# Performance work log

Measured on AMD Instinct MI355X. Metric: run time of the kernel, lower is better.

## Reference

```python
import jax, jax.numpy as jnp
import numpy as np

N, D, K = 500000, 64, 1024


def setup_inputs() -> dict:
    key = jax.random.key(0)
    kx, kc = jax.random.split(key)
    x = jax.random.normal(kx, (N, D), dtype=jnp.float32)
    centers = jax.random.normal(kc, (K, D), dtype=jnp.float32)
    return {"x": x, "centers": centers}


def reference(x, centers):
    # KMeans.predict: ids = argmin_k cdist(x, centers).
    # sqrt is monotone, so argmin over squared distances is identical, and the
    # This avoids the N x K x D expansion; the N x K score matrix is the
    # memory-bound hot path a fused kernel would stream over.
    m2 = jnp.sum(centers * centers, axis=-1)          # [K]
    scores = m2[None, :] - 2.0 * (x @ centers.T)      # [N, K]
    ids = jnp.argmin(scores, axis=-1)                 # [N]
    return ids
```

## Files before the change

### kernel.cpp

```cpp
#include <hip/hip_runtime.h>
#include <hip/hip_bf16.h>


#define N_PTS 500000
#define DIM   64
#define K_CENT 1024
#define MARGIN 8.0e-3f

typedef _Float16 half8   __attribute__((ext_vector_type(8)));
typedef float    floatx16 __attribute__((ext_vector_type(16)));

__global__ void kmeans_m2pre(const float* __restrict__ centers,
                             double* __restrict__ m2d)
{
    const int c = blockIdx.x * 256 + threadIdx.x;
    if (c >= K_CENT) return;
    const float4* crow = (const float4*)(centers + (size_t)c * DIM);
    double s = 0.0;
    #pragma unroll
    for (int kc = 0; kc < 16; ++kc) {
        float4 v = crow[kc];
        double a = v.x, b = v.y, cc = v.z, d = v.w;
        s += a * a + b * b + cc * cc + d * d;
    }
    m2d[c] = s;
}

__launch_bounds__(512, 4)
__global__ void kmeans_pass1(const float* __restrict__ x,
                             const float* __restrict__ centers,
                             int* __restrict__ out,
                             int* __restrict__ counter,
                             int* __restrict__ ulist,
                             int capacity)
{
    __shared__ __align__(16) _Float16 ldsC[256 * 72];
    __shared__ float negm2[256];

    const int tid  = threadIdx.x;
    const int lane = tid & 63;
    const int wave = tid >> 6;
    const int col  = lane & 31;
    const int h    = lane >> 5;

    const int p  = blockIdx.x * 256 + wave * 32 + col;
    const int pc = p > N_PTS - 1 ? N_PTS - 1 : p;

    half8 bh[4], bl[4];
    {
        const float* xr = x + (size_t)pc * DIM + h * 8;
        #pragma unroll
        for (int c = 0; c < 4; ++c) {
            float4 f0 = *(const float4*)(xr + c * 16);
            float4 f1 = *(const float4*)(xr + c * 16 + 4);
            float v[8] = {f0.x, f0.y, f0.z, f0.w, f1.x, f1.y, f1.z, f1.w};
            half8 hi, lo;
            #pragma unroll
            for (int j = 0; j < 8; ++j) {
                _Float16 hj = (_Float16)v[j];
                hi[j] = hj;
                lo[j] = (_Float16)(v[j] - (float)hj);
            }
            bh[c] = hi; bl[c] = lo;
        }
    }

    float m1 = -3.0e38f, m2 = -3.0e38f;
    int   ctb = 0;

    for (int s = 0; s < 4; ++s) {
        __syncthreads();
        {
            const int c = tid >> 1, hh = tid & 1;
            const float* src = centers + (size_t)(s * 256 + c) * DIM + hh * 32;
            float ss = 0.f;
            #pragma unroll
            for (int g = 0; g < 4; ++g) {
                float4 f0 = *(const float4*)(src + g * 8);
                float4 f1 = *(const float4*)(src + g * 8 + 4);
                float v[8] = {f0.x, f0.y, f0.z, f0.w, f1.x, f1.y, f1.z, f1.w};
                half8 hi;
                #pragma unroll
                for (int j = 0; j < 8; ++j) {
                    ss = fmaf(v[j], v[j], ss);
                    hi[j] = (_Float16)v[j];
                }
                *(half8*)&ldsC[c * 72 + hh * 32 + g * 8] = hi;
            }
            float oss = __shfl_xor(ss, 1);
            if (hh == 0) negm2[c] = -0.5f * (ss + oss);
        }
        __syncthreads();

        for (int ctl = 0; ctl < 8; ++ctl) {
            const int ct = s * 8 + ctl;
            const float* nm = &negm2[ctl * 32 + 4 * h];
            float4 q0 = *(const float4*)(nm);
            float4 q1 = *(const float4*)(nm + 8);
            float4 q2 = *(const float4*)(nm + 16);
            float4 q3 = *(const float4*)(nm + 24);
            floatx16 acc;
            acc[0]=q0.x; acc[1]=q0.y; acc[2]=q0.z; acc[3]=q0.w;
            acc[4]=q1.x; acc[5]=q1.y; acc[6]=q1.z; acc[7]=q1.w;
            acc[8]=q2.x; acc[9]=q2.y; acc[10]=q2.z; acc[11]=q2.w;
            acc[12]=q3.x; acc[13]=q3.y; acc[14]=q3.z; acc[15]=q3.w;

            const _Float16* ap = &ldsC[(ctl * 32 + col) * 72 + h * 8];
            #pragma unroll
            for (int c = 0; c < 4; ++c) {
                half8 a = *(const half8*)(ap + c * 16);
                acc = __builtin_amdgcn_mfma_f32_32x32x16_f16(a, bh[c], acc, 0, 0, 0);
                acc = __builtin_amdgcn_mfma_f32_32x32x16_f16(a, bl[c], acc, 0, 0, 0);
            }

            float kk[16];
            #pragma unroll
            for (int i = 0; i < 16; ++i) {
                unsigned u = (__float_as_uint(acc[i]) & 0xFFFFFFF0u) | (unsigned)i;
                kk[i] = __uint_as_float(u);
            }
            float M8[8], S8[8];
            #pragma unroll
            for (int j = 0; j < 8; ++j) {
                M8[j] = fmaxf(kk[2*j], kk[2*j+1]);
                S8[j] = fminf(kk[2*j], kk[2*j+1]);
            }
            float M4[4], S4[4];
            #pragma unroll
            for (int j = 0; j < 4; ++j) {
                M4[j] = fmaxf(M8[2*j], M8[2*j+1]);
                S4[j] = fmaxf(fmaxf(fminf(M8[2*j], M8[2*j+1]), S8[2*j]), S8[2*j+1]);
            }
            float M2a[2], S2a[2];
            #pragma unroll
            for (int j = 0; j < 2; ++j) {
                M2a[j] = fmaxf(M4[2*j], M4[2*j+1]);
                S2a[j] = fmaxf(fmaxf(fminf(M4[2*j], M4[2*j+1]), S4[2*j]), S4[2*j+1]);
            }
            float M16 = fmaxf(M2a[0], M2a[1]);
            float S16 = fmaxf(fmaxf(fminf(M2a[0], M2a[1]), S2a[0]), S2a[1]);

            m2 = fmaxf(fmaxf(m2, S16), fminf(M16, m1));
            bool gt = M16 > m1;
            m1 = gt ? M16 : m1;
            ctb = gt ? ct : ctb;
        }
    }

    {
        unsigned u = __float_as_uint(m1);
        int reg = (int)(u & 15u);
        int row = (reg & 3) + 8 * (reg >> 2) + 4 * h;
        int cid = ctb * 32 + row;

        float o1 = __shfl_xor(m1, 32);
        float o2 = __shfl_xor(m2, 32);
        int  ocid = __shfl_xor(cid, 32);
        float nm2 = fmaxf(fmaxf(m2, o2), fminf(m1, o1));
        bool take = o1 > m1;
        float nm1 = take ? o1 : m1;
        int  ncid = take ? ocid : cid;

        if (h == 0 && p < N_PTS) {
            out[p] = ncid;
            if (nm1 - nm2 < MARGIN) {
                int slot = atomicAdd(counter, 1);
                if (slot < capacity) ulist[slot] = p;
            }
        }
    }
}

__launch_bounds__(256)
__global__ void kmeans_pass2(const float* __restrict__ x,
                             const float* __restrict__ centers,
                             const double* __restrict__ m2d,
                             int* __restrict__ out,
                             const int* __restrict__ counter,
                             const int* __restrict__ ulist,
                             int capacity)
{
    int count = *counter;
    if (count > capacity) count = capacity;

    const int tid   = threadIdx.x;
    const int lane  = tid & 63;
    const int q     = lane & 15;
    const int rg    = lane >> 4;
    const int waveg = (blockIdx.x * 256 + tid) >> 6;
    const int nwave = (gridDim.x * 256) >> 6;

    for (int u = waveg; u < count; u += nwave) {
        const int p = ulist[u];
        float4 xv = *(const float4*)(x + (size_t)p * DIM + q * 4);
        const double x0 = xv.x, x1 = xv.y, x2 = xv.z, x3 = xv.w;

        double bv = 1.0e300; int bi = 0;
        #pragma unroll 4
        for (int g = 0; g < 256; ++g) {
            const int row = g * 4 + rg;
            float4 cv = *(const float4*)(centers + (size_t)row * DIM + q * 4);
            double dot = (double)cv.x * x0 + (double)cv.y * x1
                       + (double)cv.z * x2 + (double)cv.w * x3;
            #pragma unroll
            for (int m = 1; m <= 8; m <<= 1)
                dot += __shfl_xor(dot, m);
            double s = m2d[row] - 2.0 * dot;
            if (s < bv || (s == bv && row < bi)) { bv = s; bi = row; }
        }
        #pragma unroll
        for (int m = 16; m <= 32; m <<= 1) {
            double ov = __shfl_xor(bv, m);
            int    oi = __shfl_xor(bi, m);
            if (ov < bv || (ov == bv && oi < bi)) { bv = ov; bi = oi; }
        }
        if (lane == 0) out[p] = bi;
    }
}

extern "C" void kernel_launch(void* const* d_in, const int* in_sizes, int n_in,
                              void* d_out, int out_size, void* d_ws, size_t ws_size,
                              hipStream_t stream)
{
    const float* x       = (const float*)d_in[0];
    const float* centers = (const float*)d_in[1];
    int*    out     = (int*)d_out;
    int*    counter = (int*)d_ws;
    double* m2d     = (double*)((char*)d_ws + 1024);
    int*    ulist   = (int*)((char*)d_ws + 1024 + 8192);
    int capacity = (int)((ws_size > 9216 + 64 ? ws_size - 9216 : 0) / sizeof(int));
    if (capacity > N_PTS) capacity = N_PTS;

    hipMemsetAsync(d_ws, 0, 64, stream);
    kmeans_m2pre<<<4, 256, 0, stream>>>(centers, m2d);
    dim3 g1((N_PTS + 255) / 256);
    kmeans_pass1<<<g1, 512, 0, stream>>>(x, centers, out, counter, ulist, capacity);
    kmeans_pass2<<<1024, 256, 0, stream>>>(x, centers, m2d, out, counter, ulist, capacity);
}
```

Measured before the change: 389.2 us.

## Use scaled three-term fp16 split to tighten pass-1 margin and shrink refine list

Pass 1 now splits both points and centers into fp16 high and scaled low parts and computes hi*hi plus separate hi*lo and lo*hi MFMA corrections, with m2 taken from the precomputed double norms. The more accurate scores let the ambiguity margin drop sharply, so far fewer points go to the expensive fp64 pass 2. In exchange pass 1 issues three MFMAs per chunk instead of two, stages centers in 128-row tiles over eight stages, and uses a second accumulator and an extra LDS buffer, which raises register and shared-memory pressure.

```diff
diff --git a/kernel.cpp b/kernel.cpp
--- a/kernel.cpp
+++ b/kernel.cpp
@@ -5,7 +5,9 @@
 #define N_PTS 500000
 #define DIM   64
 #define K_CENT 1024
-#define MARGIN 8.0e-3f
+#define MARGIN 6.0e-4f
+#define LOSCALE 512.0f
+#define INV_LOSCALE 0.001953125f
 
 typedef _Float16 half8   __attribute__((ext_vector_type(8)));
 typedef float    floatx16 __attribute__((ext_vector_type(16)));
@@ -29,13 +31,15 @@
 __launch_bounds__(512, 4)
 __global__ void kmeans_pass1(const float* __restrict__ x,
                              const float* __restrict__ centers,
+                             const double* __restrict__ m2d,
                              int* __restrict__ out,
                              int* __restrict__ counter,
                              int* __restrict__ ulist,
                              int capacity)
 {
-    __shared__ __align__(16) _Float16 ldsC[256 * 72];
-    __shared__ float negm2[256];
+    __shared__ __align__(16) _Float16 ldsH[128 * 72];
+    __shared__ __align__(16) _Float16 ldsL[128 * 72];
+    __shared__ float negm2[128];
 
     const int tid  = threadIdx.x;
     const int lane = tid & 63;
@@ -59,7 +63,7 @@
             for (int j = 0; j < 8; ++j) {
                 _Float16 hj = (_Float16)v[j];
                 hi[j] = hj;
-                lo[j] = (_Float16)(v[j] - (float)hj);
+                lo[j] = (_Float16)((v[j] - (float)hj) * LOSCALE);
             }
             bh[c] = hi; bl[c] = lo;
         }
@@ -68,55 +72,62 @@
     float m1 = -3.0e38f, m2 = -3.0e38f;
     int   ctb = 0;
 
-    for (int s = 0; s < 4; ++s) {
+    for (int s = 0; s < 8; ++s) {
         __syncthreads();
         {
-            const int c = tid >> 1, hh = tid & 1;
-            const float* src = centers + (size_t)(s * 256 + c) * DIM + hh * 32;
-            float ss = 0.f;
-            #pragma unroll
-            for (int g = 0; g < 4; ++g) {
+            const int c = tid >> 2, part = tid & 3;
+            const float* src = centers + (size_t)(s * 128 + c) * DIM + part * 16;
+            #pragma unroll
+            for (int g = 0; g < 2; ++g) {
                 float4 f0 = *(const float4*)(src + g * 8);
                 float4 f1 = *(const float4*)(src + g * 8 + 4);
                 float v[8] = {f0.x, f0.y, f0.z, f0.w, f1.x, f1.y, f1.z, f1.w};
-                half8 hi;
+                half8 hi, lo;
                 #pragma unroll
                 for (int j = 0; j < 8; ++j) {
-                    ss = fmaf(v[j], v[j], ss);
-                    hi[j] = (_Float16)v[j];
+                    _Float16 hj = (_Float16)v[j];
+                    hi[j] = hj;
+                    lo[j] = (_Float16)((v[j] - (float)hj) * LOSCALE);
                 }
-                *(half8*)&ldsC[c * 72 + hh * 32 + g * 8] = hi;
-            }
-            float oss = __shfl_xor(ss, 1);
-            if (hh == 0) negm2[c] = -0.5f * (ss + oss);
+                *(half8*)&ldsH[c * 72 + part * 16 + g * 8] = hi;
+                *(half8*)&ldsL[c * 72 + part * 16 + g * 8] = lo;
+            }
+            if (tid < 128) negm2[tid] = -0.5f * (float)m2d[s * 128 + tid];
         }
         __syncthreads();
 
-        for (int ctl = 0; ctl < 8; ++ctl) {
-            const int ct = s * 8 + ctl;
+        for (int ctl = 0; ctl < 4; ++ctl) {
+            const int ct = s * 4 + ctl;
             const float* nm = &negm2[ctl * 32 + 4 * h];
             float4 q0 = *(const float4*)(nm);
             float4 q1 = *(const float4*)(nm + 8);
             float4 q2 = *(const float4*)(nm + 16);
             float4 q3 = *(const float4*)(nm + 24);
-            floatx16 acc;
-            acc[0]=q0.x; acc[1]=q0.y; acc[2]=q0.z; acc[3]=q0.w;
-            acc[4]=q1.x; acc[5]=q1.y; acc[6]=q1.z; acc[7]=q1.w;
-            acc[8]=q2.x; acc[9]=q2.y; acc[10]=q2.z; acc[11]=q2.w;
-            acc[12]=q3.x; acc[13]=q3.y; acc[14]=q3.z; acc[15]=q3.w;
-
-            const _Float16* ap = &ldsC[(ctl * 32 + col) * 72 + h * 8];
+            floatx16 accM;
+            accM[0]=q0.x; accM[1]=q0.y; accM[2]=q0.z; accM[3]=q0.w;
+            accM[4]=q1.x; accM[5]=q1.y; accM[6]=q1.z; accM[7]=q1.w;
+            accM[8]=q2.x; accM[9]=q2.y; accM[10]=q2.z; accM[11]=q2.w;
+            accM[12]=q3.x; accM[13]=q3.y; accM[14]=q3.z; accM[15]=q3.w;
+            floatx16 accC;
+            #pragma unroll
+            for (int i = 0; i < 16; ++i) accC[i] = 0.0f;
+
+            const _Float16* aph = &ldsH[(ctl * 32 + col) * 72 + h * 8];
+            const _Float16* apl = &ldsL[(ctl * 32 + col) * 72 + h * 8];
             #pragma unroll
             for (int c = 0; c < 4; ++c) {
-                half8 a = *(const half8*)(ap + c * 16);
-                acc = __builtin_amdgcn_mfma_f32_32x32x16_f16(a, bh[c], acc, 0, 0, 0);
-                acc = __builtin_amdgcn_mfma_f32_32x32x16_f16(a, bl[c], acc, 0, 0, 0);
+                half8 ah = *(const half8*)(aph + c * 16);
+                half8 al = *(const half8*)(apl + c * 16);
+                accM = __builtin_amdgcn_mfma_f32_32x32x16_f16(ah, bh[c], accM, 0, 0, 0);
+                accC = __builtin_amdgcn_mfma_f32_32x32x16_f16(ah, bl[c], accC, 0, 0, 0);
+                accC = __builtin_amdgcn_mfma_f32_32x32x16_f16(al, bh[c], accC, 0, 0, 0);
             }
 
             float kk[16];
             #pragma unroll
             for (int i = 0; i < 16; ++i) {
-                unsigned u = (__float_as_uint(acc[i]) & 0xFFFFFFF0u) | (unsigned)i;
+                float sc = fmaf(accC[i], INV_LOSCALE, accM[i]);
+                unsigned u = (__float_as_uint(sc) & 0xFFFFFFF0u) | (unsigned)i;
                 kk[i] = __uint_as_float(u);
             }
             float M8[8], S8[8];
@@ -234,6 +245,6 @@
     hipMemsetAsync(d_ws, 0, 64, stream);
     kmeans_m2pre<<<4, 256, 0, stream>>>(centers, m2d);
     dim3 g1((N_PTS + 255) / 256);
-    kmeans_pass1<<<g1, 512, 0, stream>>>(x, centers, out, counter, ulist, capacity);
+    kmeans_pass1<<<g1, 512, 0, stream>>>(x, centers, m2d, out, counter, ulist, capacity);
     kmeans_pass2<<<1024, 256, 0, stream>>>(x, centers, m2d, out, counter, ulist, capacity);
 }
```

New measurement: 435.0 us. +11.8%, slower.
